# Kernel optimization log

Hardware: AMD Instinct MI355X
Metric: run time of the kernel (lower is better)

The kernel has to match this reference:

```python
import jax, jax.numpy as jnp
import numpy as np

D_K = 32  # hard-coded in original module


def setup_inputs() -> dict:
    key = jax.random.key(0)
    kq, kk, kv, km = jax.random.split(key, 4)
    B, H, S, D = 4, 12, 2048, D_K
    Q = jax.random.normal(kq, (B, H, S, D), dtype=jnp.float32)
    K = jax.random.normal(kk, (B, H, S, D), dtype=jnp.float32)
    V = jax.random.normal(kv, (B, H, S, D), dtype=jnp.float32)
    attn_mask = jax.random.bernoulli(km, 0.5, (B, H, S, S))
    return {"Q": Q, "K": K, "V": V, "attn_mask": attn_mask}


def tanh_max(a):
    # (exp(a) - exp(-a)) / sum_over_keys(exp(a) + exp(-a))
    ea = jnp.exp(a)
    ena = jnp.exp(-a)
    return (ea - ena) / (ea + ena).sum(axis=-1, keepdims=True)


def reference(Q, K, V, attn_mask):
    # scores: [B,H,S,S]
    scores = jnp.einsum("bhqd,bhkd->bhqk", Q, K) / np.sqrt(D_K).astype(np.float32)
    attn = tanh_max(scores)
    # NOTE: original calls attn.masked_fill(attn_mask, 0.0) WITHOUT assignment
    # (non-in-place), so the mask has no effect. Reproduced faithfully.
    context = jnp.einsum("bhqk,bhkd->bhqd", attn, V)
    return context
```

## Files before the change

kernel.cpp:

```cpp
#include <hip/hip_runtime.h>
#include <hip/hip_bf16.h>
#include <cstdint>
#include <cstddef>


#define SLEN 2048
#define DK   32
#define NBH  48
#define PROW 40
#define NCH  32

typedef __attribute__((ext_vector_type(8))) short bf16x8;
typedef __attribute__((ext_vector_type(4))) float f32x4;

__device__ __forceinline__ unsigned pk2(float a, float b) {
    __hip_bfloat162 h = __float22bfloat162_rn(make_float2(a, b));
    union { __hip_bfloat162 h2; unsigned u; } cv; cv.h2 = h; return cv.u;
}

__global__ __launch_bounds__(256)
void prep_kv(const float* __restrict__ K, const float* __restrict__ V,
             unsigned short* __restrict__ Kbf, unsigned short* __restrict__ VTf) {
    if (blockIdx.x < NBH * 32) {
        const int b  = blockIdx.x;
        const int bh = b >> 5, kg = b & 31;
        const int tl = threadIdx.x >> 6, l = threadIdx.x & 63;
        const int t  = kg * 4 + tl;
        const int c  = t >> 1, tb = t & 1;
        const int key = c * 32 + 2 * (l & 15) + tb;
        const float* src = K + ((size_t)bh * SLEN + key) * DK + (l >> 4) * 8;
        float4 a = *(const float4*)src;
        float4 b4 = *(const float4*)(src + 4);
        union { uint4 q; unsigned u[4]; } o;
        o.u[0] = pk2(a.x, a.y);  o.u[1] = pk2(a.z, a.w);
        o.u[2] = pk2(b4.x, b4.y); o.u[3] = pk2(b4.z, b4.w);
        *(uint4*)(Kbf + (((size_t)bh * 128 + t) * 64 + l) * 8) = o.q;
    } else {
        __shared__ float tile[32][33];
        const int b  = blockIdx.x - NBH * 32;
        const int bh = b >> 6, c = b & 63;
        const int t  = threadIdx.x;
        {
            const int row = t >> 3, c4 = (t & 7) * 4;
            float4 v4 = *(const float4*)(V + ((size_t)bh * SLEN + c * 32 + row) * DK + c4);
            tile[row][c4 + 0] = v4.x; tile[row][c4 + 1] = v4.y;
            tile[row][c4 + 2] = v4.z; tile[row][c4 + 3] = v4.w;
        }
        __syncthreads();
        const int h = t >> 7, l = (t >> 1) & 63, jh = t & 1;
        const int col = h * 16 + (l & 15);
        const int r0  = (l >> 4) * 8 + jh * 4;
        uint2 u;
        u.x = pk2(tile[r0 + 0][col], tile[r0 + 1][col]);
        u.y = pk2(tile[r0 + 2][col], tile[r0 + 3][col]);
        *(uint2*)(VTf + ((((size_t)bh * 64 + c) * 2 + h) * 64 + l) * 8 + jh * 4) = u;
    }
}

__global__ __launch_bounds__(256, 6)
void attn_mfma(const float* __restrict__ Q, const unsigned short* __restrict__ Kbf,
               const unsigned short* __restrict__ VTf, float* __restrict__ Out) {
    __shared__ __align__(16) unsigned short Pbuf[4][2][16 * PROW];
    __shared__ __align__(16) float Red[2][64][12];

    const int tid  = threadIdx.x;
    const int lane = tid & 63;
    const int wv   = tid >> 6;
    const int quad = lane >> 4;
    const int l16  = lane & 15;
    const int qi   = wv >> 1;
    const int kh   = wv & 1;

    const int b   = blockIdx.x;
    const int xcd = b & 7;
    const int i   = b >> 3;
    const int bh  = xcd * 6 + (i % 6);
    const int qp  = i / 6;
    const int qbase = (qp * 2 + qi) * 16;

    const float sc = 0.17677669529663687f * 1.4426950408889634f;
    const float* qp_ = Q + ((size_t)bh * SLEN + qbase + l16) * DK + quad * 8;
    float4 qa = *(const float4*)qp_;
    float4 qb = *(const float4*)(qp_ + 4);
    union { bf16x8 v; unsigned u[4]; } aQ;
    aQ.u[0] = pk2(qa.x * sc, qa.y * sc); aQ.u[1] = pk2(qa.z * sc, qa.w * sc);
    aQ.u[2] = pk2(qb.x * sc, qb.y * sc); aQ.u[3] = pk2(qb.z * sc, qb.w * sc);

    const bf16x8* kf = (const bf16x8*)Kbf + (size_t)bh * 8192 + (size_t)kh * 4096 + lane;
    const bf16x8* vf = (const bf16x8*)VTf + (size_t)bh * 8192 + (size_t)kh * 4096 + lane;

    f32x4 o0 = {0.f, 0.f, 0.f, 0.f};
    f32x4 o1 = {0.f, 0.f, 0.f, 0.f};
    f32x4 den = {0.f, 0.f, 0.f, 0.f};
    const f32x4 zero = {0.f, 0.f, 0.f, 0.f};

    unsigned short* pb  = &Pbuf[wv][0][0];
    unsigned*       pbw = (unsigned*)pb;

    auto exppack = [&](const f32x4& s0, const f32x4& s1, int buf) {
        unsigned* pw = pbw + buf * (16 * PROW / 2);
        #pragma unroll
        for (int r = 0; r < 4; ++r) {
            float e0  = __builtin_amdgcn_exp2f(s0[r]);
            float en0 = __builtin_amdgcn_exp2f(-s0[r]);
            float e1  = __builtin_amdgcn_exp2f(s1[r]);
            float en1 = __builtin_amdgcn_exp2f(-s1[r]);
            den[r] += (e0 + en0) + (e1 + en1);
            pw[(quad * 4 + r) * (PROW / 2) + l16] = pk2(e0 - en0, e1 - en1);
        }
    };
    auto readP = [&](int buf) -> bf16x8 {
        return *(const bf16x8*)(pb + buf * (16 * PROW) + l16 * PROW + quad * 8);
    };

    bf16x8 ka = kf[0], kb = kf[64];
    f32x4 s0 = __builtin_amdgcn_mfma_f32_16x16x32_bf16(aQ.v, ka, zero, 0, 0, 0);
    f32x4 s1 = __builtin_amdgcn_mfma_f32_16x16x32_bf16(aQ.v, kb, zero, 0, 0, 0);
    ka = kf[128]; kb = kf[192];
    exppack(s0, s1, 0);

    for (int c = 0; c < NCH - 1; ++c) {
        s0 = __builtin_amdgcn_mfma_f32_16x16x32_bf16(aQ.v, ka, zero, 0, 0, 0);
        s1 = __builtin_amdgcn_mfma_f32_16x16x32_bf16(aQ.v, kb, zero, 0, 0, 0);
        const int c2 = (c + 2) & (NCH - 1);
        ka = kf[(size_t)c2 * 128]; kb = kf[(size_t)c2 * 128 + 64];
        bf16x8 vc0 = vf[(size_t)c * 128];
        bf16x8 vc1 = vf[(size_t)c * 128 + 64];
        bf16x8 aP = readP(c & 1);
        exppack(s0, s1, (c + 1) & 1);
        o0 = __builtin_amdgcn_mfma_f32_16x16x32_bf16(aP, vc0, o0, 0, 0, 0);
        o1 = __builtin_amdgcn_mfma_f32_16x16x32_bf16(aP, vc1, o1, 0, 0, 0);
    }
    {
        bf16x8 aP = readP((NCH - 1) & 1);
        bf16x8 vc0 = vf[(size_t)(NCH - 1) * 128];
        bf16x8 vc1 = vf[(size_t)(NCH - 1) * 128 + 64];
        o0 = __builtin_amdgcn_mfma_f32_16x16x32_bf16(aP, vc0, o0, 0, 0, 0);
        o1 = __builtin_amdgcn_mfma_f32_16x16x32_bf16(aP, vc1, o1, 0, 0, 0);
    }

    #pragma unroll
    for (int r = 0; r < 4; ++r) {
        den[r] += __shfl_xor(den[r], 1, 16);
        den[r] += __shfl_xor(den[r], 2, 16);
        den[r] += __shfl_xor(den[r], 4, 16);
        den[r] += __shfl_xor(den[r], 8, 16);
    }

    if (kh == 1) {
        float* r = &Red[qi][lane][0];
        *(f32x4*)(r + 0) = o0;
        *(f32x4*)(r + 4) = o1;
        *(f32x4*)(r + 8) = den;
    }
    __syncthreads();
    if (kh == 0) {
        const float* r = &Red[qi][lane][0];
        f32x4 p0 = *(const f32x4*)(r + 0);
        f32x4 p1 = *(const f32x4*)(r + 4);
        f32x4 pd = *(const f32x4*)(r + 8);
        o0 += p0; o1 += p1; den += pd;

        float* outp = Out + ((size_t)bh * SLEN + qbase) * DK;
        #pragma unroll
        for (int rr = 0; rr < 4; ++rr) {
            float inv = 1.0f / den[rr];
            int q = quad * 4 + rr;
            outp[(size_t)q * DK + l16]      = o0[rr] * inv;
            outp[(size_t)q * DK + 16 + l16] = o1[rr] * inv;
        }
    }
}

extern "C" void kernel_launch(void* const* d_in, const int* in_sizes, int n_in,
                              void* d_out, int out_size, void* d_ws, size_t ws_size,
                              hipStream_t stream) {
    const float* Q = (const float*)d_in[0];
    const float* K = (const float*)d_in[1];
    const float* V = (const float*)d_in[2];
    float* Out = (float*)d_out;
    unsigned short* Kbf = (unsigned short*)d_ws;
    unsigned short* VTf = Kbf + (size_t)NBH * SLEN * DK;

    prep_kv<<<dim3(NBH * 32 + NBH * 64), dim3(256), 0, stream>>>(K, V, Kbf, VTf);
    attn_mfma<<<dim3(3072), dim3(256), 0, stream>>>(Q, Kbf, VTf, Out);
}
```

Measured before the change: 928.9 us.

## Give each wave full key range for its own query tile, drop cross-wave reduction

Each wave now handles a distinct 16-query tile over all 2048 keys instead of two waves splitting keys for one tile. This removes the LDS partial-sum reduction and the block barrier, and halves the grid to 1536 blocks. The main loop is also unrolled by two with constant byte offsets for K/V and the P double buffer, to cut address arithmetic. In exchange each wave runs a loop twice as long with less parallelism per query tile, and there are fewer blocks to hide latency.

```diff
diff --git a/kernel.cpp b/kernel.cpp
--- a/kernel.cpp
+++ b/kernel.cpp
@@ -8,7 +8,6 @@
 #define DK   32
 #define NBH  48
 #define PROW 40
-#define NCH  32
 
 typedef __attribute__((ext_vector_type(8))) short bf16x8;
 typedef __attribute__((ext_vector_type(4))) float f32x4;
@@ -61,22 +60,19 @@
 void attn_mfma(const float* __restrict__ Q, const unsigned short* __restrict__ Kbf,
                const unsigned short* __restrict__ VTf, float* __restrict__ Out) {
     __shared__ __align__(16) unsigned short Pbuf[4][2][16 * PROW];
-    __shared__ __align__(16) float Red[2][64][12];
 
     const int tid  = threadIdx.x;
     const int lane = tid & 63;
     const int wv   = tid >> 6;
     const int quad = lane >> 4;
     const int l16  = lane & 15;
-    const int qi   = wv >> 1;
-    const int kh   = wv & 1;
 
     const int b   = blockIdx.x;
     const int xcd = b & 7;
     const int i   = b >> 3;
     const int bh  = xcd * 6 + (i % 6);
-    const int qp  = i / 6;
-    const int qbase = (qp * 2 + qi) * 16;
+    const int qg  = i / 6;
+    const int qbase = (qg * 4 + wv) * 16;
 
     const float sc = 0.17677669529663687f * 1.4426950408889634f;
     const float* qp_ = Q + ((size_t)bh * SLEN + qbase + l16) * DK + quad * 8;
@@ -86,19 +82,18 @@
     aQ.u[0] = pk2(qa.x * sc, qa.y * sc); aQ.u[1] = pk2(qa.z * sc, qa.w * sc);
     aQ.u[2] = pk2(qb.x * sc, qb.y * sc); aQ.u[3] = pk2(qb.z * sc, qb.w * sc);
 
-    const bf16x8* kf = (const bf16x8*)Kbf + (size_t)bh * 8192 + (size_t)kh * 4096 + lane;
-    const bf16x8* vf = (const bf16x8*)VTf + (size_t)bh * 8192 + (size_t)kh * 4096 + lane;
+    const char* kp = (const char*)Kbf + ((size_t)bh * 8192 + lane) * 16;
+    const char* vp = (const char*)VTf + ((size_t)bh * 8192 + lane) * 16;
 
-    f32x4 o0 = {0.f, 0.f, 0.f, 0.f};
-    f32x4 o1 = {0.f, 0.f, 0.f, 0.f};
+    f32x4 o0  = {0.f, 0.f, 0.f, 0.f};
+    f32x4 o1  = {0.f, 0.f, 0.f, 0.f};
     f32x4 den = {0.f, 0.f, 0.f, 0.f};
     const f32x4 zero = {0.f, 0.f, 0.f, 0.f};
 
-    unsigned short* pb  = &Pbuf[wv][0][0];
-    unsigned*       pbw = (unsigned*)pb;
+    unsigned* pw = (unsigned*)&Pbuf[wv][0][0] + (quad * 4) * (PROW / 2) + l16;
+    const unsigned short* pr = &Pbuf[wv][0][0] + l16 * PROW + quad * 8;
 
-    auto exppack = [&](const f32x4& s0, const f32x4& s1, int buf) {
-        unsigned* pw = pbw + buf * (16 * PROW / 2);
+    auto exppack = [&](const f32x4& s0, const f32x4& s1, const int dwofs) {
         #pragma unroll
         for (int r = 0; r < 4; ++r) {
             float e0  = __builtin_amdgcn_exp2f(s0[r]);
@@ -106,37 +101,60 @@
             float e1  = __builtin_amdgcn_exp2f(s1[r]);
             float en1 = __builtin_amdgcn_exp2f(-s1[r]);
             den[r] += (e0 + en0) + (e1 + en1);
-            pw[(quad * 4 + r) * (PROW / 2) + l16] = pk2(e0 - en0, e1 - en1);
+            pw[dwofs + r * (PROW / 2)] = pk2(e0 - en0, e1 - en1);
         }
     };
-    auto readP = [&](int buf) -> bf16x8 {
-        return *(const bf16x8*)(pb + buf * (16 * PROW) + l16 * PROW + quad * 8);
+    auto readP = [&](const int byteofs) -> bf16x8 {
+        return *(const bf16x8*)((const char*)pr + byteofs);
     };
 
-    bf16x8 ka = kf[0], kb = kf[64];
+    bf16x8 ka = *(const bf16x8*)(kp);
+    bf16x8 kb = *(const bf16x8*)(kp + 1024);
     f32x4 s0 = __builtin_amdgcn_mfma_f32_16x16x32_bf16(aQ.v, ka, zero, 0, 0, 0);
     f32x4 s1 = __builtin_amdgcn_mfma_f32_16x16x32_bf16(aQ.v, kb, zero, 0, 0, 0);
-    ka = kf[128]; kb = kf[192];
+    ka = *(const bf16x8*)(kp + 2048);
+    kb = *(const bf16x8*)(kp + 3072);
     exppack(s0, s1, 0);
+    kp += 4096;
 
-    for (int c = 0; c < NCH - 1; ++c) {
+    for (int it = 0; it < 31; ++it) {
         s0 = __builtin_amdgcn_mfma_f32_16x16x32_bf16(aQ.v, ka, zero, 0, 0, 0);
         s1 = __builtin_amdgcn_mfma_f32_16x16x32_bf16(aQ.v, kb, zero, 0, 0, 0);
-        const int c2 = (c + 2) & (NCH - 1);
-        ka = kf[(size_t)c2 * 128]; kb = kf[(size_t)c2 * 128 + 64];
-        bf16x8 vc0 = vf[(size_t)c * 128];
-        bf16x8 vc1 = vf[(size_t)c * 128 + 64];
-        bf16x8 aP = readP(c & 1);
-        exppack(s0, s1, (c + 1) & 1);
-        o0 = __builtin_amdgcn_mfma_f32_16x16x32_bf16(aP, vc0, o0, 0, 0, 0);
-        o1 = __builtin_amdgcn_mfma_f32_16x16x32_bf16(aP, vc1, o1, 0, 0, 0);
+        ka = *(const bf16x8*)(kp);
+        kb = *(const bf16x8*)(kp + 1024);
+        bf16x8 va0 = *(const bf16x8*)(vp);
+        bf16x8 va1 = *(const bf16x8*)(vp + 1024);
+        bf16x8 aP = readP(0);
+        exppack(s0, s1, 320);
+        o0 = __builtin_amdgcn_mfma_f32_16x16x32_bf16(aP, va0, o0, 0, 0, 0);
+        o1 = __builtin_amdgcn_mfma_f32_16x16x32_bf16(aP, va1, o1, 0, 0, 0);
+        s0 = __builtin_amdgcn_mfma_f32_16x16x32_bf16(aQ.v, ka, zero, 0, 0, 0);
+        s1 = __builtin_amdgcn_mfma_f32_16x16x32_bf16(aQ.v, kb, zero, 0, 0, 0);
+        ka = *(const bf16x8*)(kp + 2048);
+        kb = *(const bf16x8*)(kp + 3072);
+        bf16x8 vb0 = *(const bf16x8*)(vp + 2048);
+        bf16x8 vb1 = *(const bf16x8*)(vp + 3072);
+        aP = readP(1280);
+        exppack(s0, s1, 0);
+        o0 = __builtin_amdgcn_mfma_f32_16x16x32_bf16(aP, vb0, o0, 0, 0, 0);
+        o1 = __builtin_amdgcn_mfma_f32_16x16x32_bf16(aP, vb1, o1, 0, 0, 0);
+        kp += 4096; vp += 4096;
     }
+
     {
-        bf16x8 aP = readP((NCH - 1) & 1);
-        bf16x8 vc0 = vf[(size_t)(NCH - 1) * 128];
-        bf16x8 vc1 = vf[(size_t)(NCH - 1) * 128 + 64];
-        o0 = __builtin_amdgcn_mfma_f32_16x16x32_bf16(aP, vc0, o0, 0, 0, 0);
-        o1 = __builtin_amdgcn_mfma_f32_16x16x32_bf16(aP, vc1, o1, 0, 0, 0);
+        s0 = __builtin_amdgcn_mfma_f32_16x16x32_bf16(aQ.v, ka, zero, 0, 0, 0);
+        s1 = __builtin_amdgcn_mfma_f32_16x16x32_bf16(aQ.v, kb, zero, 0, 0, 0);
+        bf16x8 vt0 = *(const bf16x8*)(vp);
+        bf16x8 vt1 = *(const bf16x8*)(vp + 1024);
+        bf16x8 aP = readP(0);
+        exppack(s0, s1, 320);
+        o0 = __builtin_amdgcn_mfma_f32_16x16x32_bf16(aP, vt0, o0, 0, 0, 0);
+        o1 = __builtin_amdgcn_mfma_f32_16x16x32_bf16(aP, vt1, o1, 0, 0, 0);
+        aP = readP(1280);
+        vt0 = *(const bf16x8*)(vp + 2048);
+        vt1 = *(const bf16x8*)(vp + 3072);
+        o0 = __builtin_amdgcn_mfma_f32_16x16x32_bf16(aP, vt0, o0, 0, 0, 0);
+        o1 = __builtin_amdgcn_mfma_f32_16x16x32_bf16(aP, vt1, o1, 0, 0, 0);
     }
 
     #pragma unroll
@@ -147,28 +165,13 @@
         den[r] += __shfl_xor(den[r], 8, 16);
     }
 
-    if (kh == 1) {
-        float* r = &Red[qi][lane][0];
-        *(f32x4*)(r + 0) = o0;
-        *(f32x4*)(r + 4) = o1;
-        *(f32x4*)(r + 8) = den;
-    }
-    __syncthreads();
-    if (kh == 0) {
-        const float* r = &Red[qi][lane][0];
-        f32x4 p0 = *(const f32x4*)(r + 0);
-        f32x4 p1 = *(const f32x4*)(r + 4);
-        f32x4 pd = *(const f32x4*)(r + 8);
-        o0 += p0; o1 += p1; den += pd;
-
-        float* outp = Out + ((size_t)bh * SLEN + qbase) * DK;
-        #pragma unroll
-        for (int rr = 0; rr < 4; ++rr) {
-            float inv = 1.0f / den[rr];
-            int q = quad * 4 + rr;
-            outp[(size_t)q * DK + l16]      = o0[rr] * inv;
-            outp[(size_t)q * DK + 16 + l16] = o1[rr] * inv;
-        }
+    float* outp = Out + ((size_t)bh * SLEN + qbase) * DK;
+    #pragma unroll
+    for (int rr = 0; rr < 4; ++rr) {
+        float inv = 1.0f / den[rr];
+        int q = quad * 4 + rr;
+        outp[(size_t)q * DK + l16]      = o0[rr] * inv;
+        outp[(size_t)q * DK + 16 + l16] = o1[rr] * inv;
     }
 }
 
@@ -183,5 +186,5 @@
     unsigned short* VTf = Kbf + (size_t)NBH * SLEN * DK;
 
     prep_kv<<<dim3(NBH * 32 + NBH * 64), dim3(256), 0, stream>>>(K, V, Kbf, VTf);
-    attn_mfma<<<dim3(3072), dim3(256), 0, stream>>>(Q, Kbf, VTf, Out);
+    attn_mfma<<<dim3(1536), dim3(256), 0, stream>>>(Q, Kbf, VTf, Out);
 }
```

Measured after the change: 931.9 us. Within noise of the previous version (+0.3%).
